# Kernel optimization log

Hardware: AMD Instinct MI355X
Metric: run time of the kernel (lower is better)

The kernel has to match this reference:

```python
import jax, jax.numpy as jnp
import numpy as np
import math

GROUPS = 32
EPS = 1e-5
NUM_HEADS = 8


def group_norm(x, gamma, beta):
    # x: [B, C, T]
    B, C, T = x.shape
    xg = x.reshape(B, GROUPS, C // GROUPS, T)
    mean = xg.mean(axis=(2, 3), keepdims=True)
    var = xg.var(axis=(2, 3), keepdims=True)
    xn = (xg - mean) * jax.lax.rsqrt(var + EPS)
    return xn.reshape(B, C, T) * gamma[None, :, None] + beta[None, :, None]


def qkv_attention(qkv, num_heads):
    # qkv: [B, 3C, T]
    B, C3, T = qkv.shape
    split = C3 // (3 * num_heads)  # head dim
    q, k, v = jnp.split(qkv, 3, axis=1)
    scale = 1.0 / math.sqrt(math.sqrt(split))
    q = (q * scale).reshape(B * num_heads, split, T)
    k = (k * scale).reshape(B * num_heads, split, T)
    v = v.reshape(B * num_heads, split, T)
    w = jnp.einsum('bct,bcs->bts', q, k)
    w = jax.nn.softmax(w.astype(jnp.float32), axis=-1).astype(w.dtype)
    out = jnp.einsum('bts,bcs->bct', w, v)
    return out.reshape(B, -1, T)


def setup_inputs() -> dict:
    key = jax.random.key(0)
    ks = jax.random.split(key, 6)
    B, C, H, W = 16, 512, 32, 32
    x = jax.random.normal(ks[0], (B, C, H, W), dtype=jnp.float32)
    gamma = jnp.ones((C,), jnp.float32)
    beta = jnp.zeros((C,), jnp.float32)
    w_qkv = jax.random.normal(ks[1], (3 * C, C), jnp.float32) * (1.0 / math.sqrt(C))
    b_qkv = jax.random.normal(ks[2], (3 * C,), jnp.float32) * 0.01
    # proj is zero-initialized in the module; use small random weights so the
    # full op chain (proj + residual) is numerically exercised.
    w_proj = jax.random.normal(ks[3], (C, C), jnp.float32) * (1.0 / math.sqrt(C))
    b_proj = jax.random.normal(ks[4], (C,), jnp.float32) * 0.01
    return {"x": x, "gamma": gamma, "beta": beta, "w_qkv": w_qkv,
            "b_qkv": b_qkv, "w_proj": w_proj, "b_proj": b_proj}


def reference(x, gamma, beta, w_qkv, b_qkv, w_proj, b_proj):
    b, c = x.shape[0], x.shape[1]
    spatial = x.shape[2:]
    xf = x.reshape(b, c, -1)                     # [B, C, T]
    xn = group_norm(xf, gamma, beta)
    qkv = jnp.einsum('oc,bct->bot', w_qkv, xn) + b_qkv[None, :, None]
    h = qkv_attention(qkv, NUM_HEADS)
    h = jnp.einsum('oc,bct->bot', w_proj, h) + b_proj[None, :, None]
    # NOTE: residual uses the normalized x (x is reassigned before norm in torch code)
    return (xn + h).reshape(b, c, *spatial)
```

## Files before the change

kernel.cpp:

```cpp
#include <hip/hip_runtime.h>

typedef __attribute__((ext_vector_type(8))) short s16x8;
typedef __attribute__((ext_vector_type(8))) unsigned short u16x8;
typedef __attribute__((ext_vector_type(4))) unsigned short u16x4;
typedef __attribute__((ext_vector_type(4))) float f32x4;
typedef __attribute__((ext_vector_type(16))) float f32x16;

#define DEV static __device__ __forceinline__

DEV unsigned short f2bf(float f){
  union { float f; unsigned u; } v; v.f = f;
  unsigned u = v.u;
  return (unsigned short)((u + 0x7FFFu + ((u >> 16) & 1u)) >> 16);
}

DEV float bf2f(unsigned short b){
  union { unsigned u; float f; } v; v.u = ((unsigned)b) << 16;
  return v.f;
}

DEV unsigned cvt_pk(float lo, float hi){
  unsigned r;
  asm("v_cvt_pk_bf16_f32 %0, %1, %2" : "=v"(r) : "v"(lo), "v"(hi));
  return r;
}

DEV void pl32_swap(unsigned &d, unsigned &s){
  asm("v_permlane32_swap_b32 %0, %1" : "+v"(d), "+v"(s));
}

DEV void gload16(const void* g, void* l){
  __builtin_amdgcn_global_load_lds((const __attribute__((address_space(1))) void*)g,
                                   (__attribute__((address_space(3))) void*)l, 16, 0, 0);
}

__global__ __launch_bounds__(256) void k_gncvt(const float* __restrict__ x,
    const float* __restrict__ gamma, const float* __restrict__ beta,
    unsigned short* __restrict__ xt,
    const float* __restrict__ w_qkv, const float* __restrict__ w_proj,
    unsigned short* __restrict__ w_bf){
  __shared__ unsigned short lt[1024 * 16];
  __shared__ float red[8];
  __shared__ float sh_ms[2];
  const int bid = blockIdx.x;
  const int tid = threadIdx.x;

  if (bid >= 512){
    int i = (bid - 512) * 256 + tid;
    const float4* src = (i < 196608) ? (const float4*)w_qkv + i
                                     : (const float4*)w_proj + (i - 196608);
    float4 v = *src;
    unsigned long long p = (unsigned long long)f2bf(v.x)
                         | ((unsigned long long)f2bf(v.y) << 16)
                         | ((unsigned long long)f2bf(v.z) << 32)
                         | ((unsigned long long)f2bf(v.w) << 48);
    *(unsigned long long*)(w_bf + (size_t)i * 4) = p;
    return;
  }

  const int b = bid >> 5, g = bid & 31;
  const float* base = x + ((size_t)(b * 512 + g * 16)) * 1024;

  float4 vv[16];
  float s = 0.f, ss = 0.f;
  #pragma unroll
  for (int i = 0; i < 16; ++i){
    vv[i] = *(const float4*)(base + i * 1024 + tid * 4);
    s  += vv[i].x + vv[i].y + vv[i].z + vv[i].w;
    ss += vv[i].x * vv[i].x + vv[i].y * vv[i].y + vv[i].z * vv[i].z + vv[i].w * vv[i].w;
  }
  #pragma unroll
  for (int d = 1; d < 64; d <<= 1){ s += __shfl_xor(s, d); ss += __shfl_xor(ss, d); }
  if ((tid & 63) == 0){ red[tid >> 6] = s; red[4 + (tid >> 6)] = ss; }
  __syncthreads();
  if (tid == 0){
    float ts  = red[0] + red[1] + red[2] + red[3];
    float tss = red[4] + red[5] + red[6] + red[7];
    float mean = ts * (1.f / 16384.f);
    float var  = tss * (1.f / 16384.f) - mean * mean;
    float rstd = rsqrtf(var + 1e-5f);
    sh_ms[0] = mean; sh_ms[1] = rstd;
  }
  __syncthreads();
  const float mean = sh_ms[0], rstd = sh_ms[1];

  unsigned short vals[4][16];
  #pragma unroll
  for (int i = 0; i < 16; ++i){
    float gsc = gamma[g * 16 + i] * rstd;
    float bof = beta[g * 16 + i] - mean * gsc;
    vals[0][i] = f2bf(vv[i].x * gsc + bof);
    vals[1][i] = f2bf(vv[i].y * gsc + bof);
    vals[2][i] = f2bf(vv[i].z * gsc + bof);
    vals[3][i] = f2bf(vv[i].w * gsc + bof);
  }
  #pragma unroll
  for (int k2 = 0; k2 < 4; ++k2){
    u16x8 lo, hi;
    #pragma unroll
    for (int e = 0; e < 8; ++e){ lo[e] = vals[k2][e]; hi[e] = vals[k2][8 + e]; }
    int t = tid * 4 + k2;
    *(u16x8*)&lt[t * 16]     = lo;
    *(u16x8*)&lt[t * 16 + 8] = hi;
  }
  __syncthreads();
  unsigned short* dst = xt + ((size_t)b * 1024) * 512 + g * 16;
  #pragma unroll
  for (int j = 0; j < 8; ++j){
    int idx = j * 256 + tid;
    int t = idx >> 1, half = idx & 1;
    u16x8 v = *(const u16x8*)&lt[t * 16 + half * 8];
    *(u16x8*)(dst + (size_t)t * 512 + half * 8) = v;
  }
}

DEV void gemm_mainloop(const unsigned short* __restrict__ pA,
                       const unsigned short* __restrict__ pB,
                       unsigned short* As, unsigned short* Bs,
                       f32x4 (&acc)[4][4], int tid, int ldb){
  const int lane = tid & 63, wv = tid >> 6;
  const int wr = wv >> 1, wc = wv & 1;
  const int ro = lane & 15;
  for (int k0 = 0; k0 < 512; k0 += 64){
    #pragma unroll
    for (int it = 0; it < 4; ++it){
      int chunk = it * 256 + tid;
      int r = chunk >> 3, sb = chunk & 7;
      int soff = k0 + ((sb ^ (r & 7)) << 3);
      gload16(pA + (size_t)r * 512 + soff, As + (size_t)(it * 256 + wv * 64) * 8);
      gload16(pB + (size_t)r * ldb + soff, Bs + (size_t)(it * 256 + wv * 64) * 8);
    }
    __syncthreads();
    #pragma unroll
    for (int kk = 0; kk < 2; ++kk){
      s16x8 a[4], bb[4];
      int ko = kk * 64 + ((lane >> 4) << 4);
      #pragma unroll
      for (int i2 = 0; i2 < 4; ++i2){
        int ra = wr * 64 + i2 * 16 + ro;
        a[i2]  = *(const s16x8*)((const char*)As + ra * 128 + (ko ^ ((ra & 7) << 4)));
        int rb = wc * 64 + i2 * 16 + ro;
        bb[i2] = *(const s16x8*)((const char*)Bs + rb * 128 + (ko ^ ((rb & 7) << 4)));
      }
      __builtin_amdgcn_s_setprio(1);
      #pragma unroll
      for (int i2 = 0; i2 < 4; ++i2)
        #pragma unroll
        for (int j2 = 0; j2 < 4; ++j2)
          acc[i2][j2] = __builtin_amdgcn_mfma_f32_16x16x32_bf16(a[i2], bb[j2], acc[i2][j2], 0, 0, 0);
      __builtin_amdgcn_s_setprio(0);
    }
    __syncthreads();
  }
}

__global__ __launch_bounds__(256) void k_qkv(const unsigned short* __restrict__ W,
    const unsigned short* __restrict__ Xt, const float* __restrict__ bias,
    unsigned short* __restrict__ qkt, unsigned short* __restrict__ vbuf){
  __shared__ unsigned short As[128 * 64], Bs[128 * 64];
  const int bid = blockIdx.x;
  const int nt = bid & 7; const int tmp = bid >> 3;
  const int mt = tmp % 12, b = tmp / 12;
  const int tid = threadIdx.x;
  const unsigned short* Wt = W + (size_t)mt * 128 * 512;
  const unsigned short* Xb = Xt + ((size_t)(b * 1024) + nt * 128) * 512;
  f32x4 acc[4][4];
  #pragma unroll
  for (int i = 0; i < 4; ++i)
    #pragma unroll
    for (int j = 0; j < 4; ++j) acc[i][j] = f32x4{0.f, 0.f, 0.f, 0.f};
  const bool isv = (mt >= 8);
  if (isv) gemm_mainloop(Wt, Xb, As, Bs, acc, tid, 512);
  else     gemm_mainloop(Xb, Wt, As, Bs, acc, tid, 512);
  const int lane = tid & 63, wv = tid >> 6, wr = wv >> 1, wc = wv & 1;
  const int col = lane & 15, rq = (lane >> 4) << 2;
  if (isv){
    #pragma unroll
    for (int i = 0; i < 4; ++i){
      #pragma unroll
      for (int jj = 0; jj < 4; ++jj){
        int og = mt * 128 + wr * 64 + i * 16 + rq + jj;
        float bv = bias[og];
        unsigned short* drow = vbuf + ((size_t)(b * 512) + (og - 1024)) * 1024 + nt * 128 + wc * 64;
        #pragma unroll
        for (int j = 0; j < 4; ++j)
          drow[j * 16 + col] = f2bf(acc[i][j][jj] + bv);
      }
    }
  } else {
    #pragma unroll
    for (int i = 0; i < 4; ++i){
      #pragma unroll
      for (int jj = 0; jj < 4; ++jj){
        int tg = nt * 128 + wr * 64 + i * 16 + rq + jj;
        unsigned short* drow = qkt + ((size_t)(b * 1024) + tg) * 1024 + mt * 128 + wc * 64;
        #pragma unroll
        for (int j = 0; j < 4; ++j){
          int og = mt * 128 + wc * 64 + j * 16 + col;
          drow[j * 16 + col] = f2bf(acc[i][j][jj] + bias[og]);
        }
      }
    }
  }
}

__global__ __launch_bounds__(256, 4) void k_attn(unsigned short* __restrict__ qkt,
    const unsigned short* __restrict__ vbuf){
  __shared__ __align__(16) unsigned short smem[16384];

  const int bid = blockIdx.x;
  const int xcd = bid & 7, slot = bid >> 3;
  const int qt = slot & 7;
  const int b = slot >> 3, h = xcd;
  const int tid = threadIdx.x, lane = tid & 63, wv = tid >> 6;
  const int l31 = lane & 31, hi = lane >> 5;
  const int wq0 = qt * 128 + wv * 32;
  const float CSC = 0.125f * 1.44269504f;
  const float M0 = 8.f;

  s16x8 qf[4];
  {
    const unsigned short* qrow = qkt + ((size_t)(b * 1024) + wq0 + l31) * 1024 + h * 64 + hi * 8;
    #pragma unroll
    for (int kk = 0; kk < 4; ++kk)
      qf[kk] = *(const s16x8*)(qrow + kk * 16);
  }

  f32x16 o_acc[2];
  #pragma unroll
  for (int mi = 0; mi < 2; ++mi)
    #pragma unroll
    for (int e = 0; e < 16; ++e) o_acc[mi][e] = 0.f;
  float l_run = 0.f;

  const int r0 = tid >> 3;
  const int so = ((tid & 7) ^ (r0 & 7)) << 3;
  const unsigned short* pK = qkt + (size_t)(b * 1024) * 1024 + 512 + h * 64
                           + (size_t)r0 * 1024 + so;
  const unsigned short* pV = vbuf + ((size_t)(b * 512) + h * 64) * 1024
                           + (size_t)r0 * 1024 + so;
  const size_t IT1 = (size_t)32 * 1024;

  #define STAGE(bsel) do {                                                   \
    unsigned short* Kd = smem + (bsel) * 8192;                               \
    unsigned short* Vd = Kd + 4096;                                          \
    gload16(pK,       Kd + (size_t)(wv * 64) * 8);                           \
    gload16(pK + IT1, Kd + (size_t)(256 + wv * 64) * 8);                     \
    gload16(pV,       Vd + (size_t)(wv * 64) * 8);                           \
    gload16(pV + IT1, Vd + (size_t)(256 + wv * 64) * 8);                     \
    pK += 64 * 1024; pV += 64;                                               \
  } while (0)

  STAGE(0);
  __syncthreads();
  int cur = 0;

  for (int t = 0; t < 16; ++t){
    if (t < 15) STAGE(cur ^ 1);
    const unsigned short* Ks = smem + cur * 8192;
    const unsigned short* Vs = Ks + 4096;

    f32x16 sa[2];
    #pragma unroll
    for (int ni = 0; ni < 2; ++ni)
      #pragma unroll
      for (int e = 0; e < 16; ++e) sa[ni][e] = 0.f;
    #pragma unroll
    for (int kk = 0; kk < 4; ++kk){
      s16x8 kf[2];
      #pragma unroll
      for (int ni = 0; ni < 2; ++ni){
        int r = ni * 32 + l31;
        kf[ni] = *(const s16x8*)((const char*)Ks + r * 128 + ((kk * 32 + hi * 16) ^ ((r & 7) << 4)));
      }
      __builtin_amdgcn_s_setprio(1);
      sa[0] = __builtin_amdgcn_mfma_f32_32x32x16_bf16(kf[0], qf[kk], sa[0], 0, 0, 0);
      sa[1] = __builtin_amdgcn_mfma_f32_32x32x16_bf16(kf[1], qf[kk], sa[1], 0, 0, 0);
      __builtin_amdgcn_s_setprio(0);
    }

    float rsa = 0.f, rsb = 0.f;
    unsigned pk[2][4][2];
    #pragma unroll
    for (int ni = 0; ni < 2; ++ni)
      #pragma unroll
      for (int rr = 0; rr < 4; ++rr){
        float p0 = __builtin_amdgcn_exp2f(fmaf(sa[ni][4 * rr + 0], CSC, -M0));
        float p1 = __builtin_amdgcn_exp2f(fmaf(sa[ni][4 * rr + 1], CSC, -M0));
        float p2 = __builtin_amdgcn_exp2f(fmaf(sa[ni][4 * rr + 2], CSC, -M0));
        float p3 = __builtin_amdgcn_exp2f(fmaf(sa[ni][4 * rr + 3], CSC, -M0));
        rsa += p0 + p1;
        rsb += p2 + p3;
        pk[ni][rr][0] = cvt_pk(p0, p1);
        pk[ni][rr][1] = cvt_pk(p2, p3);
      }
    {
      union { float f; unsigned u; } ua, ub;
      ua.f = rsa + rsb; ub.u = ua.u;
      pl32_swap(ua.u, ub.u);
      l_run += ua.f + ub.f;
    }

    #pragma unroll
    for (int ks = 0; ks < 4; ++ks){
      int ni = ks >> 1, q2 = (ks & 1) * 2;
      unsigned d0 = pk[ni][q2][0],     d1 = pk[ni][q2][1];
      unsigned s0 = pk[ni][q2 + 1][0], s1 = pk[ni][q2 + 1][1];
      pl32_swap(d0, s0);
      pl32_swap(d1, s1);
      union { unsigned u[4]; s16x8 v; } pb;
      pb.u[0] = d0;
      pb.u[1] = d1;
      pb.u[2] = s0;
      pb.u[3] = s1;
      s16x8 vf[2];
      #pragma unroll
      for (int mi = 0; mi < 2; ++mi){
        int c = mi * 32 + l31;
        vf[mi] = *(const s16x8*)((const char*)Vs + c * 128 + ((ks * 32 + hi * 16) ^ ((c & 7) << 4)));
      }
      __builtin_amdgcn_s_setprio(1);
      o_acc[0] = __builtin_amdgcn_mfma_f32_32x32x16_bf16(vf[0], pb.v, o_acc[0], 0, 0, 0);
      o_acc[1] = __builtin_amdgcn_mfma_f32_32x32x16_bf16(vf[1], pb.v, o_acc[1], 0, 0, 0);
      __builtin_amdgcn_s_setprio(0);
    }

    asm volatile("s_waitcnt vmcnt(0)" ::: "memory");
    __builtin_amdgcn_sched_barrier(0);
    __syncthreads();
    cur ^= 1;
  }
  #undef STAGE

  float invl = 1.f / l_run;
  unsigned short* ow = smem + wv * 2048;
  int t = l31;
  #pragma unroll
  for (int mi = 0; mi < 2; ++mi)
    #pragma unroll
    for (int rr = 0; rr < 4; ++rr){
      int c0 = mi * 32 + 8 * rr + 4 * hi;
      unsigned d0 = cvt_pk(o_acc[mi][4 * rr + 0] * invl, o_acc[mi][4 * rr + 1] * invl);
      unsigned d1 = cvt_pk(o_acc[mi][4 * rr + 2] * invl, o_acc[mi][4 * rr + 3] * invl);
      unsigned* dst = (unsigned*)(ow + t * 64 + (c0 ^ ((t & 7) << 3)));
      dst[0] = d0; dst[1] = d1;
    }
  __syncthreads();
  unsigned short* hbase = qkt + ((size_t)(b * 1024) + wq0) * 1024 + h * 64;
  #pragma unroll
  for (int i = 0; i < 4; ++i){
    int id = i * 64 + lane;
    int tl = id >> 3, c8 = id & 7;
    u16x8 v = *(const u16x8*)(ow + tl * 64 + ((c8 ^ (tl & 7)) << 3));
    *(u16x8*)(hbase + (size_t)tl * 1024 + c8 * 8) = v;
  }
}

__global__ __launch_bounds__(256) void k_proj(const unsigned short* __restrict__ Wp,
    const unsigned short* __restrict__ Ht, const float* __restrict__ bias,
    const unsigned short* __restrict__ Xt, float* __restrict__ out){
  __shared__ __align__(16) unsigned short smem[17408];
  unsigned short* As = smem;
  unsigned short* Bs = smem + 8192;
  const int bid = blockIdx.x;
  const int nt = bid & 7, mt = (bid >> 3) & 3, b = bid >> 5;
  const int tid = threadIdx.x;
  f32x4 acc[4][4];
  #pragma unroll
  for (int i = 0; i < 4; ++i)
    #pragma unroll
    for (int j = 0; j < 4; ++j) acc[i][j] = f32x4{0.f, 0.f, 0.f, 0.f};
  gemm_mainloop(Wp + (size_t)mt * 128 * 512,
                Ht + ((size_t)(b * 1024) + nt * 128) * 1024, As, Bs, acc, tid, 1024);

  const unsigned short* xsrc = Xt + ((size_t)(b * 1024) + nt * 128) * 512 + mt * 128;
  #pragma unroll
  for (int p = 0; p < 8; ++p){
    int row = p * 16 + (tid >> 4);
    int c16 = (tid & 15) * 8;
    *(u16x8*)(smem + row * 136 + c16) = *(const u16x8*)(xsrc + (size_t)row * 512 + c16);
  }
  __syncthreads();

  const int lane = tid & 63, wv = tid >> 6, wr = wv >> 1, wc = wv & 1;
  const int col = lane & 15, rq = (lane >> 4) << 2;
  #pragma unroll
  for (int i = 0; i < 4; ++i){
    float bv[4];
    #pragma unroll
    for (int jj = 0; jj < 4; ++jj)
      bv[jj] = bias[mt * 128 + wr * 64 + i * 16 + rq + jj];
    #pragma unroll
    for (int j = 0; j < 4; ++j){
      int t_l  = wc * 64 + j * 16 + col;
      int og_l = wr * 64 + i * 16 + rq;
      u16x4 r4 = *(const u16x4*)(smem + t_l * 136 + og_l);
      #pragma unroll
      for (int jj = 0; jj < 4; ++jj){
        int og = mt * 128 + og_l + jj;
        float* orow = out + ((size_t)(b * 512) + og) * 1024 + nt * 128 + wc * 64;
        orow[j * 16 + col] = acc[i][j][jj] + bf2f(r4[jj]) + bv[jj];
      }
    }
  }
}

extern "C" void kernel_launch(void* const* d_in, const int* in_sizes, int n_in,
                              void* d_out, int out_size, void* d_ws, size_t ws_size,
                              hipStream_t stream) {
  (void)in_sizes; (void)n_in; (void)out_size; (void)ws_size;
  const float* x      = (const float*)d_in[0];
  const float* gamma  = (const float*)d_in[1];
  const float* beta   = (const float*)d_in[2];
  const float* w_qkv  = (const float*)d_in[3];
  const float* b_qkv  = (const float*)d_in[4];
  const float* w_proj = (const float*)d_in[5];
  const float* b_proj = (const float*)d_in[6];
  float* out = (float*)d_out;
  char* ws = (char*)d_ws;

  unsigned short* wq_bf = (unsigned short*)ws;
  unsigned short* wp_bf = (unsigned short*)(ws + 1572864);
  unsigned short* Xt    = (unsigned short*)(ws + 2101248);
  unsigned short* qkt   = (unsigned short*)(ws + 18878464);
  unsigned short* vbuf  = (unsigned short*)(ws + 52432896);

  k_gncvt<<<1536, 256, 0, stream>>>(x, gamma, beta, Xt, w_qkv, w_proj, wq_bf);
  k_qkv<<<1536, 256, 0, stream>>>(wq_bf, Xt, b_qkv, qkt, vbuf);
  k_attn<<<1024, 256, 0, stream>>>(qkt, vbuf);
  k_proj<<<512, 256, 0, stream>>>(wp_bf, qkt, b_proj, Xt, out);
}
```

Baseline: 118.0 us.

## Double attention block to eight waves sharing each K/V tile

The attention kernel now runs 512-thread blocks, each covering 256 query rows instead of 128. Each staged K/V tile in shared memory is reused by eight waves, halving global K/V traffic per query, and each thread issues one K load and one V load per stage instead of two. The double-buffered loop is unrolled by two so buffer offsets are compile-time constants, and the first QK MFMA starts from a zero vector rather than zeroing accumulators separately. The costs are half as many blocks in the grid and a tighter register budget from the 512×4 launch bounds.

```diff
diff --git a/kernel.cpp b/kernel.cpp
--- a/kernel.cpp
+++ b/kernel.cpp
@@ -204,17 +204,17 @@
   }
 }
 
-__global__ __launch_bounds__(256, 4) void k_attn(unsigned short* __restrict__ qkt,
+__global__ __launch_bounds__(512, 4) void k_attn(unsigned short* __restrict__ qkt,
     const unsigned short* __restrict__ vbuf){
   __shared__ __align__(16) unsigned short smem[16384];
 
   const int bid = blockIdx.x;
   const int xcd = bid & 7, slot = bid >> 3;
-  const int qt = slot & 7;
-  const int b = slot >> 3, h = xcd;
+  const int qt = slot & 3;
+  const int b = slot >> 2, h = xcd;
   const int tid = threadIdx.x, lane = tid & 63, wv = tid >> 6;
   const int l31 = lane & 31, hi = lane >> 5;
-  const int wq0 = qt * 128 + wv * 32;
+  const int wq0 = qt * 256 + wv * 32;
   const float CSC = 0.125f * 1.44269504f;
   const float M0 = 8.f;
 
@@ -225,6 +225,10 @@
     for (int kk = 0; kk < 4; ++kk)
       qf[kk] = *(const s16x8*)(qrow + kk * 16);
   }
+
+  f32x16 z16;
+  #pragma unroll
+  for (int e = 0; e < 16; ++e) z16[e] = 0.f;
 
   f32x16 o_acc[2];
   #pragma unroll
@@ -239,98 +243,107 @@
                            + (size_t)r0 * 1024 + so;
   const unsigned short* pV = vbuf + ((size_t)(b * 512) + h * 64) * 1024
                            + (size_t)r0 * 1024 + so;
-  const size_t IT1 = (size_t)32 * 1024;
 
   #define STAGE(bsel) do {                                                   \
     unsigned short* Kd = smem + (bsel) * 8192;                               \
     unsigned short* Vd = Kd + 4096;                                          \
-    gload16(pK,       Kd + (size_t)(wv * 64) * 8);                           \
-    gload16(pK + IT1, Kd + (size_t)(256 + wv * 64) * 8);                     \
-    gload16(pV,       Vd + (size_t)(wv * 64) * 8);                           \
-    gload16(pV + IT1, Vd + (size_t)(256 + wv * 64) * 8);                     \
+    gload16(pK, Kd + wv * 512);                                              \
+    gload16(pV, Vd + wv * 512);                                              \
     pK += 64 * 1024; pV += 64;                                               \
   } while (0)
 
+  #define DRAIN_BAR() do {                                                   \
+    asm volatile("s_waitcnt vmcnt(0)" ::: "memory");                         \
+    __builtin_amdgcn_sched_barrier(0);                                       \
+    __syncthreads();                                                         \
+  } while (0)
+
+  #define TILE(KOFF) do {                                                                          \
+    const unsigned short* Ks = smem + (KOFF);                                                      \
+    const unsigned short* Vs = Ks + 4096;                                                          \
+    f32x16 sa[2];                                                                                  \
+    {                          \
+      s16x8 kf0, kf1;                                                                              \
+      kf0 = *(const s16x8*)((const char*)Ks + (0 * 32 + l31) * 128 + ((hi * 16) ^ ((l31 & 7) << 4))); \
+      kf1 = *(const s16x8*)((const char*)Ks + (32 + l31) * 128 + ((hi * 16) ^ ((l31 & 7) << 4)));  \
+      __builtin_amdgcn_s_setprio(1);                                                               \
+      sa[0] = __builtin_amdgcn_mfma_f32_32x32x16_bf16(kf0, qf[0], z16, 0, 0, 0);                   \
+      sa[1] = __builtin_amdgcn_mfma_f32_32x32x16_bf16(kf1, qf[0], z16, 0, 0, 0);                   \
+      __builtin_amdgcn_s_setprio(0);                                                               \
+    }                                                                                              \
+    _Pragma("unroll")                                                                              \
+    for (int kk = 1; kk < 4; ++kk){                                                                \
+      s16x8 kf[2];                                                                                 \
+      _Pragma("unroll")                                                                            \
+      for (int ni = 0; ni < 2; ++ni){                                                              \
+        int r = ni * 32 + l31;                                                                     \
+        kf[ni] = *(const s16x8*)((const char*)Ks + r * 128 + ((kk * 32 + hi * 16) ^ ((r & 7) << 4))); \
+      }                                                                                            \
+      __builtin_amdgcn_s_setprio(1);                                                               \
+      sa[0] = __builtin_amdgcn_mfma_f32_32x32x16_bf16(kf[0], qf[kk], sa[0], 0, 0, 0);              \
+      sa[1] = __builtin_amdgcn_mfma_f32_32x32x16_bf16(kf[1], qf[kk], sa[1], 0, 0, 0);              \
+      __builtin_amdgcn_s_setprio(0);                                                               \
+    }                                                                                              \
+    float rsa = 0.f, rsb = 0.f;                                                                    \
+    unsigned pk[2][4][2];                                                                          \
+    _Pragma("unroll")                                                                              \
+    for (int ni = 0; ni < 2; ++ni)                                                                 \
+      _Pragma("unroll")                                                                            \
+      for (int rr = 0; rr < 4; ++rr){                                                              \
+        float p0 = __builtin_amdgcn_exp2f(fmaf(sa[ni][4 * rr + 0], CSC, -M0));                     \
+        float p1 = __builtin_amdgcn_exp2f(fmaf(sa[ni][4 * rr + 1], CSC, -M0));                     \
+        float p2 = __builtin_amdgcn_exp2f(fmaf(sa[ni][4 * rr + 2], CSC, -M0));                     \
+        float p3 = __builtin_amdgcn_exp2f(fmaf(sa[ni][4 * rr + 3], CSC, -M0));                     \
+        rsa += p0 + p1;                                                                            \
+        rsb += p2 + p3;                                                                            \
+        pk[ni][rr][0] = cvt_pk(p0, p1);                                                            \
+        pk[ni][rr][1] = cvt_pk(p2, p3);                                                            \
+      }                                                                                            \
+    {                                                                                              \
+      union { float f; unsigned u; } ua, ub;                                                       \
+      ua.f = rsa + rsb; ub.u = ua.u;                                                               \
+      pl32_swap(ua.u, ub.u);                                                                       \
+      l_run += ua.f + ub.f;                                                                        \
+    }                                                                                              \
+    _Pragma("unroll")                                                                              \
+    for (int ks = 0; ks < 4; ++ks){                                                                \
+      int ni = ks >> 1, q2 = (ks & 1) * 2;                                                         \
+      unsigned d0 = pk[ni][q2][0],     d1 = pk[ni][q2][1];                                         \
+      unsigned s0 = pk[ni][q2 + 1][0], s1 = pk[ni][q2 + 1][1];                                     \
+      pl32_swap(d0, s0);                                                                           \
+      pl32_swap(d1, s1);                                                                           \
+      union { unsigned u[4]; s16x8 v; } pb;                                                        \
+      pb.u[0] = d0;                                                                                \
+      pb.u[1] = d1;                                                                                \
+      pb.u[2] = s0;                                                                                \
+      pb.u[3] = s1;                                                                                \
+      s16x8 vf[2];                                                                                 \
+      _Pragma("unroll")                                                                            \
+      for (int mi = 0; mi < 2; ++mi){                                                              \
+        int c = mi * 32 + l31;                                                                     \
+        vf[mi] = *(const s16x8*)((const char*)Vs + c * 128 + ((ks * 32 + hi * 16) ^ ((c & 7) << 4))); \
+      }                                                                                            \
+      __builtin_amdgcn_s_setprio(1);                                                               \
+      o_acc[0] = __builtin_amdgcn_mfma_f32_32x32x16_bf16(vf[0], pb.v, o_acc[0], 0, 0, 0);          \
+      o_acc[1] = __builtin_amdgcn_mfma_f32_32x32x16_bf16(vf[1], pb.v, o_acc[1], 0, 0, 0);          \
+      __builtin_amdgcn_s_setprio(0);                                                               \
+    }                                                                                              \
+  } while (0)
+
   STAGE(0);
   __syncthreads();
-  int cur = 0;
-
-  for (int t = 0; t < 16; ++t){
-    if (t < 15) STAGE(cur ^ 1);
-    const unsigned short* Ks = smem + cur * 8192;
-    const unsigned short* Vs = Ks + 4096;
-
-    f32x16 sa[2];
-    #pragma unroll
-    for (int ni = 0; ni < 2; ++ni)
-      #pragma unroll
-      for (int e = 0; e < 16; ++e) sa[ni][e] = 0.f;
-    #pragma unroll
-    for (int kk = 0; kk < 4; ++kk){
-      s16x8 kf[2];
-      #pragma unroll
-      for (int ni = 0; ni < 2; ++ni){
-        int r = ni * 32 + l31;
-        kf[ni] = *(const s16x8*)((const char*)Ks + r * 128 + ((kk * 32 + hi * 16) ^ ((r & 7) << 4)));
-      }
-      __builtin_amdgcn_s_setprio(1);
-      sa[0] = __builtin_amdgcn_mfma_f32_32x32x16_bf16(kf[0], qf[kk], sa[0], 0, 0, 0);
-      sa[1] = __builtin_amdgcn_mfma_f32_32x32x16_bf16(kf[1], qf[kk], sa[1], 0, 0, 0);
-      __builtin_amdgcn_s_setprio(0);
-    }
-
-    float rsa = 0.f, rsb = 0.f;
-    unsigned pk[2][4][2];
-    #pragma unroll
-    for (int ni = 0; ni < 2; ++ni)
-      #pragma unroll
-      for (int rr = 0; rr < 4; ++rr){
-        float p0 = __builtin_amdgcn_exp2f(fmaf(sa[ni][4 * rr + 0], CSC, -M0));
-        float p1 = __builtin_amdgcn_exp2f(fmaf(sa[ni][4 * rr + 1], CSC, -M0));
-        float p2 = __builtin_amdgcn_exp2f(fmaf(sa[ni][4 * rr + 2], CSC, -M0));
-        float p3 = __builtin_amdgcn_exp2f(fmaf(sa[ni][4 * rr + 3], CSC, -M0));
-        rsa += p0 + p1;
-        rsb += p2 + p3;
-        pk[ni][rr][0] = cvt_pk(p0, p1);
-        pk[ni][rr][1] = cvt_pk(p2, p3);
-      }
-    {
-      union { float f; unsigned u; } ua, ub;
-      ua.f = rsa + rsb; ub.u = ua.u;
-      pl32_swap(ua.u, ub.u);
-      l_run += ua.f + ub.f;
-    }
-
-    #pragma unroll
-    for (int ks = 0; ks < 4; ++ks){
-      int ni = ks >> 1, q2 = (ks & 1) * 2;
-      unsigned d0 = pk[ni][q2][0],     d1 = pk[ni][q2][1];
-      unsigned s0 = pk[ni][q2 + 1][0], s1 = pk[ni][q2 + 1][1];
-      pl32_swap(d0, s0);
-      pl32_swap(d1, s1);
-      union { unsigned u[4]; s16x8 v; } pb;
-      pb.u[0] = d0;
-      pb.u[1] = d1;
-      pb.u[2] = s0;
-      pb.u[3] = s1;
-      s16x8 vf[2];
-      #pragma unroll
-      for (int mi = 0; mi < 2; ++mi){
-        int c = mi * 32 + l31;
-        vf[mi] = *(const s16x8*)((const char*)Vs + c * 128 + ((ks * 32 + hi * 16) ^ ((c & 7) << 4)));
-      }
-      __builtin_amdgcn_s_setprio(1);
-      o_acc[0] = __builtin_amdgcn_mfma_f32_32x32x16_bf16(vf[0], pb.v, o_acc[0], 0, 0, 0);
-      o_acc[1] = __builtin_amdgcn_mfma_f32_32x32x16_bf16(vf[1], pb.v, o_acc[1], 0, 0, 0);
-      __builtin_amdgcn_s_setprio(0);
-    }
-
-    asm volatile("s_waitcnt vmcnt(0)" ::: "memory");
-    __builtin_amdgcn_sched_barrier(0);
-    __syncthreads();
-    cur ^= 1;
+
+  for (int tp = 0; tp < 8; ++tp){
+    STAGE(1);
+    TILE(0);
+    DRAIN_BAR();
+    if (tp < 7) STAGE(0);
+    TILE(8192);
+    DRAIN_BAR();
   }
   #undef STAGE
+  #undef TILE
+  #undef DRAIN_BAR
 
   float invl = 1.f / l_run;
   unsigned short* ow = smem + wv * 2048;
@@ -427,6 +440,6 @@
 
   k_gncvt<<<1536, 256, 0, stream>>>(x, gamma, beta, Xt, w_qkv, w_proj, wq_bf);
   k_qkv<<<1536, 256, 0, stream>>>(wq_bf, Xt, b_qkv, qkt, vbuf);
-  k_attn<<<1024, 256, 0, stream>>>(qkt, vbuf);
+  k_attn<<<512, 512, 0, stream>>>(qkt, vbuf);
   k_proj<<<512, 256, 0, stream>>>(wp_bf, qkt, b_proj, Xt, out);
 }
```

Result: faster. 114.2 us (-3.3%).
